# Optimization experiments

Measured on AMD Instinct MI355X. Metric: run time of the kernel, lower is better.

Reference implementation:

```python
import jax, jax.numpy as jnp
import numpy as np

B, L, D_MODEL = 4, 2048, 1024
D_STATE, D_CONV, EXPAND, HEADDIM = 128, 4, 2, 64
D_INNER = EXPAND * D_MODEL            # 2048
NHEADS = D_INNER // HEADDIM           # 32
CONV_DIM = D_INNER + 2 * D_STATE      # 2304
D_IN_PROJ = 2 * D_INNER + 2 * D_STATE + NHEADS  # 4448
EPS = 1e-5


def _silu(v):
    return v * jax.nn.sigmoid(v)


def setup_inputs() -> dict:
    key = jax.random.key(0)
    ks = jax.random.split(key, 8)
    x = jax.random.normal(ks[0], (B, L, D_MODEL), dtype=jnp.float32)
    ln_w = jnp.ones((D_MODEL,), jnp.float32)
    ln_b = jnp.zeros((D_MODEL,), jnp.float32)
    in_proj_w = jax.random.normal(ks[1], (D_IN_PROJ, D_MODEL), jnp.float32) * 0.02
    conv_w = jax.random.normal(ks[2], (CONV_DIM, D_CONV), jnp.float32) * 0.2
    conv_b = jnp.zeros((CONV_DIM,), jnp.float32)
    # inverse-softplus of dt sampled in [1e-3, 1e-1], matching mamba2 dt init
    dt_bias = jnp.log(jnp.expm1(jax.random.uniform(ks[3], (NHEADS,), minval=0.001, maxval=0.1)))
    # A sampled uniform in [1,16], stored as log (A = -exp(A_log))
    A_log = jnp.log(jax.random.uniform(ks[4], (NHEADS,), minval=1.0, maxval=16.0))
    D = jnp.ones((NHEADS,), jnp.float32)
    rms_w = jnp.ones((D_INNER,), jnp.float32)
    out_proj_w = jax.random.normal(ks[5], (D_MODEL, D_INNER), jnp.float32) * 0.02
    return {"x": x, "ln_w": ln_w, "ln_b": ln_b, "in_proj_w": in_proj_w,
            "conv_w": conv_w, "conv_b": conv_b, "dt_bias": dt_bias,
            "A_log": A_log, "D": D, "rms_w": rms_w, "out_proj_w": out_proj_w}


def reference(x, ln_w, ln_b, in_proj_w, conv_w, conv_b, dt_bias, A_log, D, rms_w, out_proj_w):
    b = x.shape[0]
    # LayerNorm
    mu = x.mean(-1, keepdims=True)
    var = ((x - mu) ** 2).mean(-1, keepdims=True)
    u = (x - mu) * jax.lax.rsqrt(var + EPS) * ln_w + ln_b
    # input projection -> z | xBC | dt
    zxbcdt = jnp.einsum('bld,ed->ble', u, in_proj_w)
    z = zxbcdt[..., :D_INNER]
    xBC = zxbcdt[..., D_INNER:D_INNER + CONV_DIM]
    dt = jax.nn.softplus(zxbcdt[..., -NHEADS:] + dt_bias)  # (b,l,h)
    # causal depthwise conv along time (kernel D_CONV) + silu
    xpad = jnp.pad(xBC, ((0, 0), (D_CONV - 1, 0), (0, 0)))
    conv = conv_b + sum(conv_w[:, k] * xpad[:, k:k + L, :] for k in range(D_CONV))
    xBC = _silu(conv)
    xh = xBC[..., :D_INNER].reshape(b, L, NHEADS, HEADDIM)       # (b,l,h,p)
    Bm = xBC[..., D_INNER:D_INNER + D_STATE]                      # (b,l,n)
    Cm = xBC[..., D_INNER + D_STATE:]                             # (b,l,n)
    A = -jnp.exp(A_log)                                           # (h,)
    dA = jnp.exp(dt * A)                                          # (b,l,h)
    dtx = dt[..., None] * xh                                      # (b,l,h,p)

    def step(h, inp):
        dA_t, dtx_t, B_t, C_t = inp
        h = dA_t[:, :, None, None] * h + dtx_t[..., None] * B_t[:, None, None, :]
        y_t = jnp.einsum('bhpn,bn->bhp', h, C_t)
        return h, y_t

    h0 = jnp.zeros((b, NHEADS, HEADDIM, D_STATE), x.dtype)
    xs = (dA.transpose(1, 0, 2), dtx.transpose(1, 0, 2, 3),
          Bm.transpose(1, 0, 2), Cm.transpose(1, 0, 2))
    _, ys = jax.lax.scan(step, h0, xs)                            # (l,b,h,p)
    y = ys.transpose(1, 0, 2, 3) + D[None, None, :, None] * xh    # skip term
    y = y.reshape(b, L, D_INNER)
    # gated RMSNorm: rmsnorm(y * silu(z)) * weight
    g = y * _silu(z)
    g = g * jax.lax.rsqrt((g * g).mean(-1, keepdims=True) + EPS) * rms_w
    out = jnp.einsum('ble,de->bld', g, out_proj_w)
    # residual; dropout is identity in eval mode
    return out + x
```

## Files before the change

kernel.cpp:

```cpp
#include <hip/hip_runtime.h>
#include <hip/hip_bf16.h>

#define DEV __device__ __forceinline__

typedef unsigned short u16;
typedef unsigned int u32;
typedef float f32x4 __attribute__((ext_vector_type(4)));
typedef short s16x8 __attribute__((ext_vector_type(8)));

static constexpr int Bb = 4, Ll = 2048, DM = 1024, DI = 2048, NH = 32;
static constexpr int CD = 2304;
static constexpr int NP = 4384;
static constexpr int NP_PAD = 4480;
static constexpr int BL = Bb * Ll;
static constexpr int NC = 32;

DEV float u2f(u16 s) { return __uint_as_float(((u32)s) << 16); }
DEV u16 f2bu(float f) {
  __hip_bfloat16 h = __float2bfloat16(f);
  u16 s; __builtin_memcpy(&s, &h, 2); return s;
}
DEV float blo(u32 u) { return __uint_as_float(u << 16); }
DEV float bhi(u32 u) { return __uint_as_float(u & 0xffff0000u); }

DEV int swz64(int r, int k)  { return r * 64  + ((((k >> 3) ^ (r & 7))) << 3) + (k & 7); }

DEV void gl_lds16(const u16* g, u16* l) {
  __builtin_amdgcn_global_load_lds(
      (const __attribute__((address_space(1))) u32*)g,
      (__attribute__((address_space(3))) u32*)l, 16, 0, 0);
}

__global__ __launch_bounds__(256) void cvt_pad(const float* __restrict__ src,
    u16* __restrict__ dst, int total, int cols, int realRows) {
  int i = blockIdx.x * 256 + threadIdx.x;
  if (i >= total) return;
  int r = i / cols;
  dst[i] = (r < realRows) ? f2bu(src[i]) : (u16)0;
}

__global__ __launch_bounds__(256) void ln_kernel(const float* __restrict__ x,
    const float* __restrict__ w, const float* __restrict__ bia, u16* __restrict__ u) {
  int row = blockIdx.x, tid = threadIdx.x;
  const float4* xr = (const float4*)(x + (size_t)row * DM);
  float4 v = xr[tid];
  float s = v.x + v.y + v.z + v.w;
  float s2 = v.x*v.x + v.y*v.y + v.z*v.z + v.w*v.w;
  #pragma unroll
  for (int o = 32; o; o >>= 1) { s += __shfl_down(s, o); s2 += __shfl_down(s2, o); }
  __shared__ float rs[4], rs2[4];
  int wv = tid >> 6, ln = tid & 63;
  if (ln == 0) { rs[wv] = s; rs2[wv] = s2; }
  __syncthreads();
  s = rs[0] + rs[1] + rs[2] + rs[3];
  s2 = rs2[0] + rs2[1] + rs2[2] + rs2[3];
  float mu = s * (1.f / DM);
  float var = s2 * (1.f / DM) - mu * mu;
  float inv = rsqrtf(var + 1e-5f);
  float4 wv4 = ((const float4*)w)[tid], bv4 = ((const float4*)bia)[tid];
  ushort4 o;
  o.x = f2bu((v.x - mu) * inv * wv4.x + bv4.x);
  o.y = f2bu((v.y - mu) * inv * wv4.y + bv4.y);
  o.z = f2bu((v.z - mu) * inv * wv4.z + bv4.z);
  o.w = f2bu((v.w - mu) * inv * wv4.w + bv4.w);
  ((ushort4*)(u + (size_t)row * DM))[tid] = o;
}

template<int MODE>
__global__ __launch_bounds__(256) void gemm_nt(const u16* __restrict__ A,
    const u16* __restrict__ Bw, void* __restrict__ o0, void* __restrict__ o1,
    void* __restrict__ o2, const float* __restrict__ resid, int N, int K) {
  __shared__ u16 sA[128 * 32];
  __shared__ u16 sB[128 * 32];
  int tid = threadIdx.x, wid = tid >> 6, lane = tid & 63;
  int m0 = blockIdx.x * 128, n0 = blockIdx.y * 128;
  int wm = (wid >> 1) * 64, wn = (wid & 1) * 64;
  f32x4 acc[4][4];
  #pragma unroll
  for (int i = 0; i < 4; i++)
    #pragma unroll
    for (int j = 0; j < 4; j++) acc[i][j] = (f32x4){0.f, 0.f, 0.f, 0.f};
  int rA = wid * 32 + (lane >> 2);
  int cA = (lane & 3) * 8;
  const u16* gA = A + (size_t)(m0 + rA) * K + cA;
  const u16* gB = Bw + (size_t)(n0 + rA) * K + cA;
  u16* lA0 = &sA[(wid * 2 + 0) * 512]; u16* lA1 = &sA[(wid * 2 + 1) * 512];
  u16* lB0 = &sB[(wid * 2 + 0) * 512]; u16* lB1 = &sB[(wid * 2 + 1) * 512];
  int fr = lane & 15, fk = (lane >> 4) * 8, fq = lane >> 4;
  for (int kk = 0; kk < K; kk += 32) {
    gl_lds16(gA + kk, lA0);
    gl_lds16(gA + (size_t)16 * K + kk, lA1);
    gl_lds16(gB + kk, lB0);
    gl_lds16(gB + (size_t)16 * K + kk, lB1);
    __syncthreads();
    s16x8 af[4], bfr[4];
    #pragma unroll
    for (int i = 0; i < 4; i++) af[i] = *(const s16x8*)&sA[(wm + i * 16 + fr) * 32 + fk];
    #pragma unroll
    for (int i = 0; i < 4; i++) bfr[i] = *(const s16x8*)&sB[(wn + i * 16 + fr) * 32 + fk];
    #pragma unroll
    for (int mi = 0; mi < 4; mi++)
      #pragma unroll
      for (int ni = 0; ni < 4; ni++)
        acc[mi][ni] = __builtin_amdgcn_mfma_f32_16x16x32_bf16(af[mi], bfr[ni], acc[mi][ni], 0, 0, 0);
    __syncthreads();
  }
  if (MODE == 0) {
    const int by = blockIdx.y;
    u16* ob; int ostr, cb0;
    if (by < 16)      { ob = (u16*)o0; ostr = 2048; cb0 = 0; }
    else if (by < 34) { ob = (u16*)o1; ostr = 2304; cb0 = 2048; }
    else              { ob = (u16*)o2; ostr = 32;   cb0 = 4352; }
    #pragma unroll
    for (int mi = 0; mi < 4; mi++) {
      #pragma unroll
      for (int ni = 0; ni < 4; ni++) {
        int col = n0 + wn + ni * 16 + fr;
        int c = col - cb0;
        if (by == 34 && c >= 32) continue;
        #pragma unroll
        for (int r = 0; r < 4; r++) {
          int row = m0 + wm + mi * 16 + fq * 4 + r;
          ob[(size_t)row * ostr + c] = f2bu(acc[mi][ni][r]);
        }
      }
    }
  } else {
    float* of = (float*)o0;
    #pragma unroll
    for (int mi = 0; mi < 4; mi++) {
      #pragma unroll
      for (int ni = 0; ni < 4; ni++) {
        int col = n0 + wn + ni * 16 + fr;
        #pragma unroll
        for (int r = 0; r < 4; r++) {
          int row = m0 + wm + mi * 16 + fq * 4 + r;
          of[(size_t)row * N + col] = acc[mi][ni][r] + resid[(size_t)row * N + col];
        }
      }
    }
  }
}

__global__ __launch_bounds__(256) void conv_silu(const u16* __restrict__ xbc,
    const float* __restrict__ cw, const float* __restrict__ cb, u16* __restrict__ out) {
  int i = blockIdx.x * 256 + threadIdx.x;
  if (i >= BL * CD) return;
  int c = i % CD;
  int bl = i / CD;
  int l = bl % Ll;
  float acc = cb[c];
  #pragma unroll
  for (int k = 0; k < 4; ++k) {
    int ls = l - 3 + k;
    if (ls >= 0) acc += cw[c * 4 + k] * u2f(xbc[(size_t)(bl - 3 + k) * CD + c]);
  }
  float sg = 1.f / (1.f + __expf(-acc));
  out[i] = f2bu(acc * sg);
}

__global__ __launch_bounds__(256) void dt_cumsum(const u16* __restrict__ dtraw,
    const float* __restrict__ dtb, const float* __restrict__ alog,
    float* __restrict__ dtv, float* __restrict__ sv) {
  int wid = threadIdx.x >> 6, lane = threadIdx.x & 63;
  int g = blockIdx.x * 4 + wid;
  int b = g >> 10, h = (g >> 5) & 31, c = g & 31;
  int t = c * 64 + lane;
  float raw = u2f(dtraw[(size_t)(b * Ll + t) * 32 + h]);
  float v = raw + dtb[h];
  float dt = (v > 20.f) ? v : log1pf(__expf(v));
  float a = -dt * __expf(alog[h]);
  float s = a;
  #pragma unroll
  for (int o = 1; o < 64; o <<= 1) {
    float u = __shfl_up(s, o);
    if (lane >= o) s += u;
  }
  int idx = (b * 32 + h) * Ll + t;
  dtv[idx] = dt;
  sv[idx] = s;
}

__global__ __launch_bounds__(256) void chunk_state(const u16* __restrict__ conv,
    const float* __restrict__ dtv, const float* __restrict__ sv,
    u16* __restrict__ S) {
  __shared__ u16 xsT[64 * 64];
  __shared__ u16 BT[128 * 64];
  int gid = blockIdx.x;
  int c = gid & 31, h = (gid >> 5) & 31, b = gid >> 10;
  int bh = b * 32 + h;
  int tid = threadIdx.x, w = tid >> 6, lane = tid & 63;
  int fr = lane & 15, fq = lane >> 4;
  int j = tid & 63, pg = tid >> 6;
  int tb = c * 64;
  const float* svb = sv + (size_t)bh * Ll + tb;
  const float* dvb = dtv + (size_t)bh * Ll + tb;
  const u16* cvb = conv + (size_t)(b * Ll + tb) * CD;
  float s_last = svb[63];
  float wj = __expf(s_last - svb[j]) * dvb[j];
  const u16* rowp = cvb + (size_t)j * CD;
  #pragma unroll
  for (int rep = 0; rep < 2; rep++) {
    int p0 = rep * 32 + pg * 8;
    uint4 v = *(const uint4*)(rowp + h * 64 + p0);
    u32 va[4] = {v.x, v.y, v.z, v.w};
    #pragma unroll
    for (int e = 0; e < 4; e++) {
      xsT[swz64(p0 + 2 * e, j)]     = f2bu(blo(va[e]) * wj);
      xsT[swz64(p0 + 2 * e + 1, j)] = f2bu(bhi(va[e]) * wj);
    }
  }
  #pragma unroll
  for (int rep = 0; rep < 4; rep++) {
    int n0 = rep * 32 + pg * 8;
    uint4 v = *(const uint4*)(rowp + DI + n0);
    u32 va[4] = {v.x, v.y, v.z, v.w};
    #pragma unroll
    for (int e = 0; e < 4; e++) {
      BT[swz64(n0 + 2 * e, j)]     = (u16)(va[e] & 0xffffu);
      BT[swz64(n0 + 2 * e + 1, j)] = (u16)(va[e] >> 16);
    }
  }
  __syncthreads();
  f32x4 acc[4][2];
  #pragma unroll
  for (int mi = 0; mi < 4; mi++)
    #pragma unroll
    for (int ni = 0; ni < 2; ni++) acc[mi][ni] = (f32x4){0.f, 0.f, 0.f, 0.f};
  #pragma unroll
  for (int ks = 0; ks < 2; ks++) {
    int k8 = ks * 4 + fq;
    s16x8 bfv[2];
    #pragma unroll
    for (int ni = 0; ni < 2; ni++) {
      int rb = w * 32 + ni * 16 + fr;
      bfv[ni] = *(const s16x8*)&BT[rb * 64 + ((k8 ^ (rb & 7)) << 3)];
    }
    #pragma unroll
    for (int mi = 0; mi < 4; mi++) {
      int ra = mi * 16 + fr;
      s16x8 af = *(const s16x8*)&xsT[ra * 64 + ((k8 ^ (ra & 7)) << 3)];
      #pragma unroll
      for (int ni = 0; ni < 2; ni++)
        acc[mi][ni] = __builtin_amdgcn_mfma_f32_16x16x32_bf16(af, bfv[ni], acc[mi][ni], 0, 0, 0);
    }
  }
  u16* Sc = S + (size_t)gid * 8192;
  #pragma unroll
  for (int mi = 0; mi < 4; mi++) {
    #pragma unroll
    for (int ni = 0; ni < 2; ni++) {
      int p = mi * 16 + fq * 4;
      int n = w * 32 + ni * 16 + fr;
      #pragma unroll
      for (int r = 0; r < 4; r++)
        Sc[(size_t)(p + r) * 128 + n] = f2bu(acc[mi][ni][r]);
    }
  }
}

__global__ __launch_bounds__(256) void state_pass(u16* __restrict__ S,
    const float* __restrict__ sv) {
  int bh = blockIdx.x >> 3, q = blockIdx.x & 7;
  int o = q * 1024 + threadIdx.x * 4;
  const float* svb = sv + (size_t)bh * Ll;
  u16* base = S + (size_t)bh * NC * 8192 + o;
  float acc[4] = {0.f, 0.f, 0.f, 0.f};
  for (int c = 0; c < NC; c++) {
    uint2 sc = *(const uint2*)(base + (size_t)c * 8192);
    uint2 pre;
    pre.x = (u32)f2bu(acc[0]) | ((u32)f2bu(acc[1]) << 16);
    pre.y = (u32)f2bu(acc[2]) | ((u32)f2bu(acc[3]) << 16);
    *(uint2*)(base + (size_t)c * 8192) = pre;
    float E = __expf(svb[c * 64 + 63]);
    acc[0] = E * acc[0] + blo(sc.x);
    acc[1] = E * acc[1] + bhi(sc.x);
    acc[2] = E * acc[2] + blo(sc.y);
    acc[3] = E * acc[3] + bhi(sc.y);
  }
}

__global__ __launch_bounds__(256) void chunk_out(const u16* __restrict__ conv,
    const u16* __restrict__ hstart, const float* __restrict__ dtv,
    const float* __restrict__ sv, const float* __restrict__ Dp,
    u16* __restrict__ yb) {
  __shared__ u16 Ct[64 * 128];
  __shared__ u16 Bt[64 * 128];
  __shared__ u16 Hs[64 * 128];
  __shared__ u16 xT[64 * 64];
  __shared__ u16 Ml[64 * 64];
  __shared__ float svl[64], dtl[64], pexl[64];
  int gid = blockIdx.x;
  int c = gid & 31, h = (gid >> 5) & 31, b = gid >> 10;
  int tid = threadIdx.x, w = tid >> 6, lane = tid & 63;
  int fr = lane & 15, fq = lane >> 4;
  int tb = c * 64;
  const u16* cvb = conv + ((size_t)b * Ll + tb) * CD;
  const u16* hsrc = hstart + (((size_t)(b * 32 + h)) * NC + c) * 8192;
  #pragma unroll
  for (int qq = 0; qq < 4; qq++) {
    int q = w * 4 + qq;
    int i = q * 4 + (lane >> 4);
    int s = lane & 15;
    int kc = ((s ^ (i & 7)) << 3);
    gl_lds16(cvb + (size_t)i * CD + 2176 + kc, &Ct[q * 512]);
    gl_lds16(cvb + (size_t)i * CD + 2048 + kc, &Bt[q * 512]);
    gl_lds16(hsrc + (size_t)i * 128 + kc, &Hs[q * 512]);
  }
  {
    int j = tid & 63, pg = tid >> 6;
    const u16* rowp = cvb + (size_t)j * CD + h * 64;
    #pragma unroll
    for (int rep = 0; rep < 2; rep++) {
      int p0 = rep * 32 + pg * 8;
      uint4 v = *(const uint4*)(rowp + p0);
      u32 va[4] = {v.x, v.y, v.z, v.w};
      #pragma unroll
      for (int e = 0; e < 4; e++) {
        xT[swz64(p0 + 2 * e, j)]     = (u16)(va[e] & 0xffffu);
        xT[swz64(p0 + 2 * e + 1, j)] = (u16)(va[e] >> 16);
      }
    }
  }
  if (tid < 64) {
    float s = sv[(size_t)(b * 32 + h) * Ll + tb + tid];
    svl[tid] = s;
    pexl[tid] = __expf(s);
    dtl[tid] = dtv[(size_t)(b * 32 + h) * Ll + tb + tid];
  }
  __syncthreads();
  f32x4 g2[4];
  #pragma unroll
  for (int mi = 0; mi < 4; mi++) g2[mi] = (f32x4){0.f, 0.f, 0.f, 0.f};
  int wj = w * 16;
  #pragma unroll
  for (int ks = 0; ks < 4; ks++) {
    int k8 = ks * 4 + fq;
    int rb = wj + fr;
    s16x8 bf = *(const s16x8*)&Bt[rb * 128 + ((k8 ^ (rb & 7)) << 3)];
    #pragma unroll
    for (int mi = 0; mi < 4; mi++) {
      int ra = mi * 16 + fr;
      s16x8 af = *(const s16x8*)&Ct[ra * 128 + ((k8 ^ (ra & 7)) << 3)];
      g2[mi] = __builtin_amdgcn_mfma_f32_16x16x32_bf16(af, bf, g2[mi], 0, 0, 0);
    }
  }
  #pragma unroll
  for (int mi = 0; mi < 4; mi++) {
    int jj = wj + fr;
    #pragma unroll
    for (int r = 0; r < 4; r++) {
      int ii = mi * 16 + fq * 4 + r;
      float v = 0.f;
      if (jj <= ii) v = g2[mi][r] * __expf(svl[ii] - svl[jj]) * dtl[jj];
      Ml[swz64(ii, jj)] = f2bu(v);
    }
  }
  __syncthreads();
  f32x4 aY[4], a4[4];
  #pragma unroll
  for (int mi = 0; mi < 4; mi++) { aY[mi] = (f32x4){0.f, 0.f, 0.f, 0.f}; a4[mi] = (f32x4){0.f, 0.f, 0.f, 0.f}; }
  int wp = w * 16;
  #pragma unroll
  for (int ks = 0; ks < 2; ks++) {
    int k8 = ks * 4 + fq;
    int rb = wp + fr;
    s16x8 bf = *(const s16x8*)&xT[rb * 64 + ((k8 ^ (rb & 7)) << 3)];
    #pragma unroll
    for (int mi = 0; mi < 4; mi++) {
      int ra = mi * 16 + fr;
      s16x8 af = *(const s16x8*)&Ml[ra * 64 + ((k8 ^ (ra & 7)) << 3)];
      aY[mi] = __builtin_amdgcn_mfma_f32_16x16x32_bf16(af, bf, aY[mi], 0, 0, 0);
    }
  }
  #pragma unroll
  for (int ks = 0; ks < 4; ks++) {
    int k8 = ks * 4 + fq;
    int rb = wp + fr;
    s16x8 bf = *(const s16x8*)&Hs[rb * 128 + ((k8 ^ (rb & 7)) << 3)];
    #pragma unroll
    for (int mi = 0; mi < 4; mi++) {
      int ra = mi * 16 + fr;
      s16x8 af = *(const s16x8*)&Ct[ra * 128 + ((k8 ^ (ra & 7)) << 3)];
      a4[mi] = __builtin_amdgcn_mfma_f32_16x16x32_bf16(af, bf, a4[mi], 0, 0, 0);
    }
  }
  float Dh = Dp[h];
  u16* yrow = yb + ((size_t)b * Ll + tb) * DI + h * 64;
  #pragma unroll
  for (int mi = 0; mi < 4; mi++) {
    int p = wp + fr;
    #pragma unroll
    for (int r = 0; r < 4; r++) {
      int i = mi * 16 + fq * 4 + r;
      float xh = u2f(xT[swz64(p, i)]);
      yrow[(size_t)i * DI + p] = f2bu(aY[mi][r] + pexl[i] * a4[mi][r] + Dh * xh);
    }
  }
}

__global__ __launch_bounds__(256) void gate_rms(const u16* __restrict__ y,
    const u16* __restrict__ zbuf, const float* __restrict__ rw, u16* __restrict__ g) {
  int bl = blockIdx.x, tid = threadIdx.x;
  uint4 yv = ((const uint4*)(y + (size_t)bl * DI))[tid];
  uint4 zv = ((const uint4*)(zbuf + (size_t)bl * DI))[tid];
  u32 ya[4] = {yv.x, yv.y, yv.z, yv.w};
  u32 za[4] = {zv.x, zv.y, zv.z, zv.w};
  float gv[8];
  float ss = 0.f;
  #pragma unroll
  for (int jx = 0; jx < 4; jx++) {
    float y0 = blo(ya[jx]), y1 = bhi(ya[jx]);
    float z0 = blo(za[jx]), z1 = bhi(za[jx]);
    float s0 = z0 / (1.f + __expf(-z0));
    float s1 = z1 / (1.f + __expf(-z1));
    gv[jx * 2] = y0 * s0; gv[jx * 2 + 1] = y1 * s1;
    ss += gv[jx * 2] * gv[jx * 2] + gv[jx * 2 + 1] * gv[jx * 2 + 1];
  }
  #pragma unroll
  for (int o = 32; o; o >>= 1) ss += __shfl_down(ss, o);
  __shared__ float red[4];
  int wv = tid >> 6, ln = tid & 63;
  if (ln == 0) red[wv] = ss;
  __syncthreads();
  ss = red[0] + red[1] + red[2] + red[3];
  float scale = rsqrtf(ss * (1.f / DI) + 1e-5f);
  const float* rwp = rw + tid * 8;
  ushort4 o0, o1;
  o0.x = f2bu(gv[0] * scale * rwp[0]); o0.y = f2bu(gv[1] * scale * rwp[1]);
  o0.z = f2bu(gv[2] * scale * rwp[2]); o0.w = f2bu(gv[3] * scale * rwp[3]);
  o1.x = f2bu(gv[4] * scale * rwp[4]); o1.y = f2bu(gv[5] * scale * rwp[5]);
  o1.z = f2bu(gv[6] * scale * rwp[6]); o1.w = f2bu(gv[7] * scale * rwp[7]);
  ushort4* gp = (ushort4*)(g + (size_t)bl * DI + tid * 8);
  gp[0] = o0; gp[1] = o1;
}

extern "C" void kernel_launch(void* const* d_in, const int* in_sizes, int n_in,
                              void* d_out, int out_size, void* d_ws, size_t ws_size,
                              hipStream_t stream) {
  const float* x    = (const float*)d_in[0];
  const float* lnw  = (const float*)d_in[1];
  const float* lnb  = (const float*)d_in[2];
  const float* w1   = (const float*)d_in[3];
  const float* cw   = (const float*)d_in[4];
  const float* cb   = (const float*)d_in[5];
  const float* dtb  = (const float*)d_in[6];
  const float* alog = (const float*)d_in[7];
  const float* Dp   = (const float*)d_in[8];
  const float* rw   = (const float*)d_in[9];
  const float* w2   = (const float*)d_in[10];

  char* ws = (char*)d_ws;
  u16*   ub     = (u16*)(ws + 0);
  u16*   W1b    = (u16*)(ws + 16777216);
  u16*   conv   = (u16*)(ws + 0);
  u16*   zbuf   = (u16*)(ws + 37748736);
  u16*   xbc    = (u16*)(ws + 71303168);
  u16*   dtraw  = (u16*)(ws + 109051904);
  u16*   Sbuf   = (u16*)(ws + 71303168);
  u16*   gb     = (u16*)(ws + 71303168);
  float* dtv    = (float*)(ws + 138412032);
  float* sv     = (float*)(ws + 139460608);
  u16*   yb     = (u16*)(ws + 140509184);
  u16*   W2b    = (u16*)(ws + 174063616);
  if (ws_size < 178257920u) return;

  float* out = (float*)d_out;

  cvt_pad<<<(NP_PAD * 1024) / 256, 256, 0, stream>>>(w1, W1b, NP_PAD * 1024, 1024, NP);
  cvt_pad<<<(1024 * 2048) / 256, 256, 0, stream>>>(w2, W2b, 1024 * 2048, 2048, 1024);
  ln_kernel<<<BL, 256, 0, stream>>>(x, lnw, lnb, ub);
  gemm_nt<0><<<dim3(64, 35), 256, 0, stream>>>(ub, W1b, zbuf, xbc, dtraw, nullptr, NP, 1024);
  conv_silu<<<(BL * CD) / 256, 256, 0, stream>>>(xbc, cw, cb, conv);
  dt_cumsum<<<1024, 256, 0, stream>>>(dtraw, dtb, alog, dtv, sv);
  chunk_state<<<4096, 256, 0, stream>>>(conv, dtv, sv, Sbuf);
  state_pass<<<1024, 256, 0, stream>>>(Sbuf, sv);
  chunk_out<<<4096, 256, 0, stream>>>(conv, Sbuf, dtv, sv, Dp, yb);
  gate_rms<<<BL, 256, 0, stream>>>(yb, zbuf, rw, gb);
  gemm_nt<1><<<dim3(64, 8), 256, 0, stream>>>(gb, W2b, out, nullptr, nullptr, x, 1024, 2048);
}
```

Measured before the change: 383.7 us.

## Replace input projection GEMM with 256x256 double-buffered swizzled-LDS kernel

The input projection GEMM becomes a dedicated kernel with 256x256 tiles and 8 waves per block. It double-buffers 64-wide K slabs into XOR-swizzled LDS through direct global-to-LDS loads, overlapping loads with MFMA work through fine-grained waitcnt and barrier phases. It also remaps blocks for L2 locality and raises wave priority around the MFMA bursts. The weight padding grows to a multiple of 256 rows, and output routing to z, xBC and dt moves to per-column checks; the larger tile gives about 1.1 waves of blocks on the device.

```diff
diff --git a/kernel.cpp b/kernel.cpp
--- a/kernel.cpp
+++ b/kernel.cpp
@@ -11,7 +11,7 @@
 static constexpr int Bb = 4, Ll = 2048, DM = 1024, DI = 2048, NH = 32;
 static constexpr int CD = 2304;
 static constexpr int NP = 4384;
-static constexpr int NP_PAD = 4480;
+static constexpr int NP_PAD = 4608;
 static constexpr int BL = Bb * Ll;
 static constexpr int NC = 32;
 
@@ -66,10 +66,120 @@
   ((ushort4*)(u + (size_t)row * DM))[tid] = o;
 }
 
-template<int MODE>
-__global__ __launch_bounds__(256) void gemm_nt(const u16* __restrict__ A,
-    const u16* __restrict__ Bw, void* __restrict__ o0, void* __restrict__ o1,
-    void* __restrict__ o2, const float* __restrict__ resid, int N, int K) {
+__global__ __launch_bounds__(512, 2) void gemm_in8(const u16* __restrict__ A,
+    const u16* __restrict__ Bw, u16* __restrict__ zbuf, u16* __restrict__ xbc,
+    u16* __restrict__ dtraw) {
+  __shared__ u16 SH[65536];
+  int tid = threadIdx.x, wid = tid >> 6, lane = tid & 63;
+  int fr = lane & 15, fq = lane >> 4;
+  int nb = blockIdx.y * 32 + blockIdx.x;
+  int s = (nb & 7) * 72 + (nb >> 3);
+  int m0 = (s & 31) * 256;
+  int n0 = (s >> 5) * 256;
+  int wm = (wid >> 2) * 128, wn = (wid & 3) * 64;
+  int lrow = lane >> 3;
+  int ksrcE = (((lane & 7) * 16) ^ (lrow << 4)) >> 1;
+
+  f32x4 acc[8][4];
+  #pragma unroll
+  for (int i = 0; i < 8; i++)
+    #pragma unroll
+    for (int j = 0; j < 4; j++) acc[i][j] = (f32x4){0.f, 0.f, 0.f, 0.f};
+
+  auto STAGE = [&](const u16* gbase, int rowOrigin, int shElem, int t, int h) {
+    #pragma unroll
+    for (int q = 0; q < 2; q++) {
+      int r0 = h * 128 + q * 64 + wid * 8;
+      const u16* src = gbase + (size_t)(rowOrigin + r0 + lrow) * 1024 + t * 64 + ksrcE;
+      gl_lds16(src, &SH[shElem + r0 * 64]);
+    }
+  };
+
+  STAGE(A, m0, 0, 0, 0);
+  STAGE(A, m0, 0, 0, 1);
+  STAGE(Bw, n0, 32768, 0, 0);
+  STAGE(Bw, n0, 32768, 0, 1);
+
+  s16x8 bB[2][4];
+  for (int it = 0; it < 8; it++) {
+    #pragma unroll
+    for (int p = 0; p < 8; p++) {
+      if (p < 4) {
+        int u = 2 * it + 1;
+        if (p == 0) STAGE(A, m0, 16384, u, 0);
+        if (p == 1) STAGE(A, m0, 16384, u, 1);
+        if (p == 2) STAGE(Bw, n0, 32768 + 16384, u, 0);
+        if (p == 3) STAGE(Bw, n0, 32768 + 16384, u, 1);
+      } else if (it < 7) {
+        int v = 2 * it + 2;
+        if (p == 4) STAGE(A, m0, 0, v, 0);
+        if (p == 5) STAGE(A, m0, 0, v, 1);
+        if (p == 6) STAGE(Bw, n0, 32768, v, 0);
+        if (p == 7) STAGE(Bw, n0, 32768, v, 1);
+      }
+      if (p == 0) {
+        asm volatile("s_waitcnt vmcnt(2)\n\ts_barrier" ::: "memory");
+      } else if (p == 4) {
+        if (it < 7) asm volatile("s_waitcnt vmcnt(2)\n\ts_barrier" ::: "memory");
+        else        asm volatile("s_waitcnt vmcnt(0)\n\ts_barrier" ::: "memory");
+      } else {
+        asm volatile("s_barrier" ::: "memory");
+      }
+      int buf = p >> 2;
+      int ab = buf * 16384, bb = 32768 + buf * 16384;
+      if (p == 0 || p == 4) {
+        #pragma unroll
+        for (int nf = 0; nf < 4; nf++)
+          #pragma unroll
+          for (int ks = 0; ks < 2; ks++) {
+            int rb = wn + nf * 16 + fr;
+            bB[ks][nf] = *(const s16x8*)&SH[bb + rb * 64 +
+                ((((ks * 64 + fq * 16) ^ ((rb & 7) << 4))) >> 1)];
+          }
+      }
+      int q = p & 3;
+      s16x8 af[2][2];
+      #pragma unroll
+      for (int ml = 0; ml < 2; ml++)
+        #pragma unroll
+        for (int ks = 0; ks < 2; ks++) {
+          int ra = wm + q * 32 + ml * 16 + fr;
+          af[ml][ks] = *(const s16x8*)&SH[ab + ra * 64 +
+              ((((ks * 64 + fq * 16) ^ ((ra & 7) << 4))) >> 1)];
+        }
+      __builtin_amdgcn_s_setprio(1);
+      #pragma unroll
+      for (int ml = 0; ml < 2; ml++)
+        #pragma unroll
+        for (int nf = 0; nf < 4; nf++)
+          #pragma unroll
+          for (int ks = 0; ks < 2; ks++)
+            acc[q * 2 + ml][nf] = __builtin_amdgcn_mfma_f32_16x16x32_bf16(
+                af[ml][ks], bB[ks][nf], acc[q * 2 + ml][nf], 0, 0, 0);
+      __builtin_amdgcn_s_setprio(0);
+      asm volatile("s_barrier" ::: "memory");
+    }
+  }
+  #pragma unroll
+  for (int mf = 0; mf < 8; mf++) {
+    #pragma unroll
+    for (int nf = 0; nf < 4; nf++) {
+      int col = n0 + wn + nf * 16 + fr;
+      #pragma unroll
+      for (int r = 0; r < 4; r++) {
+        int row = m0 + wm + mf * 16 + fq * 4 + r;
+        float v = acc[mf][nf][r];
+        if (col < 2048)       zbuf[(size_t)row * 2048 + col] = f2bu(v);
+        else if (col < 4352)  xbc[(size_t)row * 2304 + (col - 2048)] = f2bu(v);
+        else if (col < 4384)  dtraw[(size_t)row * 32 + (col - 4352)] = f2bu(v);
+      }
+    }
+  }
+}
+
+__global__ __launch_bounds__(256) void gemm_out(const u16* __restrict__ A,
+    const u16* __restrict__ Bw, float* __restrict__ of,
+    const float* __restrict__ resid, int N, int K) {
   __shared__ u16 sA[128 * 32];
   __shared__ u16 sB[128 * 32];
   int tid = threadIdx.x, wid = tid >> 6, lane = tid & 63;
@@ -105,38 +215,15 @@
         acc[mi][ni] = __builtin_amdgcn_mfma_f32_16x16x32_bf16(af[mi], bfr[ni], acc[mi][ni], 0, 0, 0);
     __syncthreads();
   }
-  if (MODE == 0) {
-    const int by = blockIdx.y;
-    u16* ob; int ostr, cb0;
-    if (by < 16)      { ob = (u16*)o0; ostr = 2048; cb0 = 0; }
-    else if (by < 34) { ob = (u16*)o1; ostr = 2304; cb0 = 2048; }
-    else              { ob = (u16*)o2; ostr = 32;   cb0 = 4352; }
-    #pragma unroll
-    for (int mi = 0; mi < 4; mi++) {
-      #pragma unroll
-      for (int ni = 0; ni < 4; ni++) {
-        int col = n0 + wn + ni * 16 + fr;
-        int c = col - cb0;
-        if (by == 34 && c >= 32) continue;
-        #pragma unroll
-        for (int r = 0; r < 4; r++) {
-          int row = m0 + wm + mi * 16 + fq * 4 + r;
-          ob[(size_t)row * ostr + c] = f2bu(acc[mi][ni][r]);
-        }
-      }
-    }
-  } else {
-    float* of = (float*)o0;
-    #pragma unroll
-    for (int mi = 0; mi < 4; mi++) {
-      #pragma unroll
-      for (int ni = 0; ni < 4; ni++) {
-        int col = n0 + wn + ni * 16 + fr;
-        #pragma unroll
-        for (int r = 0; r < 4; r++) {
-          int row = m0 + wm + mi * 16 + fq * 4 + r;
-          of[(size_t)row * N + col] = acc[mi][ni][r] + resid[(size_t)row * N + col];
-        }
+  #pragma unroll
+  for (int mi = 0; mi < 4; mi++) {
+    #pragma unroll
+    for (int ni = 0; ni < 4; ni++) {
+      int col = n0 + wn + ni * 16 + fr;
+      #pragma unroll
+      for (int r = 0; r < 4; r++) {
+        int row = m0 + wm + mi * 16 + fq * 4 + r;
+        of[(size_t)row * N + col] = acc[mi][ni][r] + resid[(size_t)row * N + col];
       }
     }
   }
@@ -470,12 +557,12 @@
   cvt_pad<<<(NP_PAD * 1024) / 256, 256, 0, stream>>>(w1, W1b, NP_PAD * 1024, 1024, NP);
   cvt_pad<<<(1024 * 2048) / 256, 256, 0, stream>>>(w2, W2b, 1024 * 2048, 2048, 1024);
   ln_kernel<<<BL, 256, 0, stream>>>(x, lnw, lnb, ub);
-  gemm_nt<0><<<dim3(64, 35), 256, 0, stream>>>(ub, W1b, zbuf, xbc, dtraw, nullptr, NP, 1024);
+  gemm_in8<<<dim3(32, 18), 512, 0, stream>>>(ub, W1b, zbuf, xbc, dtraw);
   conv_silu<<<(BL * CD) / 256, 256, 0, stream>>>(xbc, cw, cb, conv);
   dt_cumsum<<<1024, 256, 0, stream>>>(dtraw, dtb, alog, dtv, sv);
   chunk_state<<<4096, 256, 0, stream>>>(conv, dtv, sv, Sbuf);
   state_pass<<<1024, 256, 0, stream>>>(Sbuf, sv);
   chunk_out<<<4096, 256, 0, stream>>>(conv, Sbuf, dtv, sv, Dp, yb);
   gate_rms<<<BL, 256, 0, stream>>>(yb, zbuf, rw, gb);
-  gemm_nt<1><<<dim3(64, 8), 256, 0, stream>>>(gb, W2b, out, nullptr, nullptr, x, 1024, 2048);
-}
+  gemm_out<<<dim3(64, 8), 256, 0, stream>>>(gb, W2b, out, x, 1024, 2048);
+}
```

Result: slower. 416.1 us (+8.4%).

## Rewrite input GEMM with double-buffered swizzled LDS, XCD mapping; vectorize conv

Applied to the files above, without the earlier changes.

Replaces the input-projection GEMM with a 512-thread kernel using 256x128 tiles, double-buffered LDS staging with an XOR swizzle to avoid bank conflicts, XCD-aware block ordering for L2 locality, and s_setprio around the MFMA loop. The output GEMM becomes a separate non-templated kernel. The conv+silu kernel now handles 8 channels per thread with 16-byte loads and stores. This targets LDS bank conflicts, load latency exposure and narrow memory accesses, at the cost of higher LDS and register use per block.

```diff
diff --git a/kernel.cpp b/kernel.cpp
--- a/kernel.cpp
+++ b/kernel.cpp
@@ -66,10 +66,86 @@
   ((ushort4*)(u + (size_t)row * DM))[tid] = o;
 }
 
-template<int MODE>
-__global__ __launch_bounds__(256) void gemm_nt(const u16* __restrict__ A,
-    const u16* __restrict__ Bw, void* __restrict__ o0, void* __restrict__ o1,
-    void* __restrict__ o2, const float* __restrict__ resid, int N, int K) {
+__global__ __launch_bounds__(512, 4) void gemm_in8(const u16* __restrict__ A,
+    const u16* __restrict__ Bw, u16* __restrict__ zbuf, u16* __restrict__ xbc,
+    u16* __restrict__ dtraw) {
+  __shared__ u16 SH[24576];
+  int tid = threadIdx.x, wid = tid >> 6, lane = tid & 63;
+  int fr = lane & 15, fq = lane >> 4;
+  int nb = blockIdx.x;
+  int xcd = nb & 7, i = nb >> 3;
+  int m0 = (xcd * 4 + (i & 3)) * 256;
+  int n0 = (i >> 2) * 128;
+  int wm = (wid >> 1) * 64, wn = (wid & 1) * 64;
+  int ksrcE = (((lane & 3) ^ ((lane >> 3) & 3)) << 3);
+  int lr = lane >> 2;
+
+  f32x4 acc[4][4];
+  #pragma unroll
+  for (int a = 0; a < 4; a++)
+    #pragma unroll
+    for (int b = 0; b < 4; b++) acc[a][b] = (f32x4){0.f, 0.f, 0.f, 0.f};
+
+  auto STGA = [&](int t, int dstE) {
+    #pragma unroll
+    for (int h = 0; h < 2; h++) {
+      int r0 = h * 128 + wid * 16;
+      gl_lds16(A + (size_t)(m0 + r0 + lr) * 1024 + t * 32 + ksrcE, &SH[dstE + r0 * 32]);
+    }
+  };
+  auto STGB = [&](int t, int dstE) {
+    int r0 = wid * 16;
+    gl_lds16(Bw + (size_t)(n0 + r0 + lr) * 1024 + t * 32 + ksrcE, &SH[dstE + r0 * 32]);
+  };
+
+  STGA(0, 0);
+  STGB(0, 16384);
+  asm volatile("s_waitcnt vmcnt(0)" ::: "memory");
+  __builtin_amdgcn_s_barrier();
+  for (int t = 0; t < 32; t++) {
+    int ca = (t & 1) * 8192, cbf = 16384 + (t & 1) * 4096;
+    if (t < 31) {
+      STGA(t + 1, ((t + 1) & 1) * 8192);
+      STGB(t + 1, 16384 + ((t + 1) & 1) * 4096);
+    }
+    s16x8 bB[4];
+    #pragma unroll
+    for (int nf = 0; nf < 4; nf++) {
+      int rb = wn + nf * 16 + fr;
+      bB[nf] = *(const s16x8*)&SH[cbf + rb * 32 + ((fq ^ ((rb >> 1) & 3)) << 3)];
+    }
+    __builtin_amdgcn_s_setprio(1);
+    #pragma unroll
+    for (int mf = 0; mf < 4; mf++) {
+      int ra = wm + mf * 16 + fr;
+      s16x8 af = *(const s16x8*)&SH[ca + ra * 32 + ((fq ^ ((ra >> 1) & 3)) << 3)];
+      #pragma unroll
+      for (int nf = 0; nf < 4; nf++)
+        acc[mf][nf] = __builtin_amdgcn_mfma_f32_16x16x32_bf16(af, bB[nf], acc[mf][nf], 0, 0, 0);
+    }
+    __builtin_amdgcn_s_setprio(0);
+    __syncthreads();
+  }
+  #pragma unroll
+  for (int mf = 0; mf < 4; mf++) {
+    #pragma unroll
+    for (int nf = 0; nf < 4; nf++) {
+      int col = n0 + wn + nf * 16 + fr;
+      #pragma unroll
+      for (int r = 0; r < 4; r++) {
+        int row = m0 + wm + mf * 16 + fq * 4 + r;
+        float v = acc[mf][nf][r];
+        if (col < 2048)       zbuf[(size_t)row * 2048 + col] = f2bu(v);
+        else if (col < 4352)  xbc[(size_t)row * 2304 + (col - 2048)] = f2bu(v);
+        else if (col < 4384)  dtraw[(size_t)row * 32 + (col - 4352)] = f2bu(v);
+      }
+    }
+  }
+}
+
+__global__ __launch_bounds__(256) void gemm_out(const u16* __restrict__ A,
+    const u16* __restrict__ Bw, float* __restrict__ of,
+    const float* __restrict__ resid, int N, int K) {
   __shared__ u16 sA[128 * 32];
   __shared__ u16 sB[128 * 32];
   int tid = threadIdx.x, wid = tid >> 6, lane = tid & 63;
@@ -105,38 +181,15 @@
         acc[mi][ni] = __builtin_amdgcn_mfma_f32_16x16x32_bf16(af[mi], bfr[ni], acc[mi][ni], 0, 0, 0);
     __syncthreads();
   }
-  if (MODE == 0) {
-    const int by = blockIdx.y;
-    u16* ob; int ostr, cb0;
-    if (by < 16)      { ob = (u16*)o0; ostr = 2048; cb0 = 0; }
-    else if (by < 34) { ob = (u16*)o1; ostr = 2304; cb0 = 2048; }
-    else              { ob = (u16*)o2; ostr = 32;   cb0 = 4352; }
-    #pragma unroll
-    for (int mi = 0; mi < 4; mi++) {
-      #pragma unroll
-      for (int ni = 0; ni < 4; ni++) {
-        int col = n0 + wn + ni * 16 + fr;
-        int c = col - cb0;
-        if (by == 34 && c >= 32) continue;
-        #pragma unroll
-        for (int r = 0; r < 4; r++) {
-          int row = m0 + wm + mi * 16 + fq * 4 + r;
-          ob[(size_t)row * ostr + c] = f2bu(acc[mi][ni][r]);
-        }
-      }
-    }
-  } else {
-    float* of = (float*)o0;
-    #pragma unroll
-    for (int mi = 0; mi < 4; mi++) {
-      #pragma unroll
-      for (int ni = 0; ni < 4; ni++) {
-        int col = n0 + wn + ni * 16 + fr;
-        #pragma unroll
-        for (int r = 0; r < 4; r++) {
-          int row = m0 + wm + mi * 16 + fq * 4 + r;
-          of[(size_t)row * N + col] = acc[mi][ni][r] + resid[(size_t)row * N + col];
-        }
+  #pragma unroll
+  for (int mi = 0; mi < 4; mi++) {
+    #pragma unroll
+    for (int ni = 0; ni < 4; ni++) {
+      int col = n0 + wn + ni * 16 + fr;
+      #pragma unroll
+      for (int r = 0; r < 4; r++) {
+        int row = m0 + wm + mi * 16 + fq * 4 + r;
+        of[(size_t)row * N + col] = acc[mi][ni][r] + resid[(size_t)row * N + col];
       }
     }
   }
@@ -145,18 +198,39 @@
 __global__ __launch_bounds__(256) void conv_silu(const u16* __restrict__ xbc,
     const float* __restrict__ cw, const float* __restrict__ cb, u16* __restrict__ out) {
   int i = blockIdx.x * 256 + threadIdx.x;
-  if (i >= BL * CD) return;
-  int c = i % CD;
-  int bl = i / CD;
-  int l = bl % Ll;
-  float acc = cb[c];
-  #pragma unroll
-  for (int k = 0; k < 4; ++k) {
+  if (i >= BL * (CD / 8)) return;
+  int c8 = i % (CD / 8);
+  int bl = i / (CD / 8);
+  int l = bl & (Ll - 1);
+  int c0 = c8 * 8;
+  uint4 R[4];
+  #pragma unroll
+  for (int k = 0; k < 4; k++) {
     int ls = l - 3 + k;
-    if (ls >= 0) acc += cw[c * 4 + k] * u2f(xbc[(size_t)(bl - 3 + k) * CD + c]);
-  }
-  float sg = 1.f / (1.f + __expf(-acc));
-  out[i] = f2bu(acc * sg);
+    if (ls >= 0) R[k] = *(const uint4*)(xbc + (size_t)(bl - 3 + k) * CD + c0);
+    else         R[k] = (uint4){0u, 0u, 0u, 0u};
+  }
+  u16 o[8];
+  #pragma unroll
+  for (int e = 0; e < 8; e++) {
+    float acc = cb[c0 + e];
+    float4 wv = *(const float4*)(cw + (size_t)(c0 + e) * 4);
+    float wk[4] = {wv.x, wv.y, wv.z, wv.w};
+    #pragma unroll
+    for (int k = 0; k < 4; k++) {
+      u32 word = (&R[k].x)[e >> 1];
+      float xv = (e & 1) ? bhi(word) : blo(word);
+      acc += wk[k] * xv;
+    }
+    float sg = 1.f / (1.f + __expf(-acc));
+    o[e] = f2bu(acc * sg);
+  }
+  uint4 ov;
+  ov.x = (u32)o[0] | ((u32)o[1] << 16);
+  ov.y = (u32)o[2] | ((u32)o[3] << 16);
+  ov.z = (u32)o[4] | ((u32)o[5] << 16);
+  ov.w = (u32)o[6] | ((u32)o[7] << 16);
+  *(uint4*)(out + (size_t)bl * CD + c0) = ov;
 }
 
 __global__ __launch_bounds__(256) void dt_cumsum(const u16* __restrict__ dtraw,
@@ -470,12 +544,12 @@
   cvt_pad<<<(NP_PAD * 1024) / 256, 256, 0, stream>>>(w1, W1b, NP_PAD * 1024, 1024, NP);
   cvt_pad<<<(1024 * 2048) / 256, 256, 0, stream>>>(w2, W2b, 1024 * 2048, 2048, 1024);
   ln_kernel<<<BL, 256, 0, stream>>>(x, lnw, lnb, ub);
-  gemm_nt<0><<<dim3(64, 35), 256, 0, stream>>>(ub, W1b, zbuf, xbc, dtraw, nullptr, NP, 1024);
-  conv_silu<<<(BL * CD) / 256, 256, 0, stream>>>(xbc, cw, cb, conv);
+  gemm_in8<<<1120, 512, 0, stream>>>(ub, W1b, zbuf, xbc, dtraw);
+  conv_silu<<<(BL * (CD / 8)) / 256, 256, 0, stream>>>(xbc, cw, cb, conv);
   dt_cumsum<<<1024, 256, 0, stream>>>(dtraw, dtb, alog, dtv, sv);
   chunk_state<<<4096, 256, 0, stream>>>(conv, dtv, sv, Sbuf);
   state_pass<<<1024, 256, 0, stream>>>(Sbuf, sv);
   chunk_out<<<4096, 256, 0, stream>>>(conv, Sbuf, dtv, sv, Dp, yb);
   gate_rms<<<BL, 256, 0, stream>>>(yb, zbuf, rw, gb);
-  gemm_nt<1><<<dim3(64, 8), 256, 0, stream>>>(gb, W2b, out, nullptr, nullptr, x, 1024, 2048);
-}
+  gemm_out<<<dim3(64, 8), 256, 0, stream>>>(gb, W2b, out, x, 1024, 2048);
+}
```

Result: faster. 338.3 us (-11.8%).
